# Performance work log

Hardware: AMD Instinct MI355X
Metric: run time of the kernel (lower is better)

## Reference

```python
import jax, jax.numpy as jnp
import numpy as np

L = 4        # num_layers
B = 32       # batch
N = 512      # num_nodes == seq_len
D = 256      # d_model
H = 8        # nhead
HD = D // H  # head_dim
F = 1024     # dim_feedforward
EPS = 1e-5


def setup_inputs() -> dict:
    key = jax.random.key(0)
    ks = jax.random.split(key, 12)
    w = lambda k, shape: jax.random.normal(k, shape, jnp.float32) * 0.02
    return {
        "src": jax.random.normal(ks[0], (B, N, D), jnp.float32),
        # node embeddings (torch.randn -> std 1)
        "e1": jax.random.normal(ks[1], (N, D), jnp.float32),
        "e2": jax.random.normal(ks[2], (N, D), jnp.float32),
        # per-layer attention projections, stored [L, d_in, d_out]
        "Wq": w(ks[3], (L, D, D)), "bq": jnp.zeros((L, D), jnp.float32),
        "Wk": w(ks[4], (L, D, D)), "bk": jnp.zeros((L, D), jnp.float32),
        "Wv": w(ks[5], (L, D, D)), "bv": jnp.zeros((L, D), jnp.float32),
        "Wo": w(ks[6], (L, D, D)), "bo": jnp.zeros((L, D), jnp.float32),
        # FFN
        "W1": w(ks[7], (L, D, F)), "b1": jnp.zeros((L, F), jnp.float32),
        "W2": w(ks[8], (L, F, D)), "b2": jnp.zeros((L, D), jnp.float32),
        # LayerNorms
        "g1": jnp.ones((L, D), jnp.float32), "be1": jnp.zeros((L, D), jnp.float32),
        "g2": jnp.ones((L, D), jnp.float32), "be2": jnp.zeros((L, D), jnp.float32),
    }


def _layernorm(x, g, b):
    mu = jnp.mean(x, axis=-1, keepdims=True)
    var = jnp.mean(jnp.square(x - mu), axis=-1, keepdims=True)
    return (x - mu) * jax.lax.rsqrt(var + EPS) * g + b


def reference(src, e1, e2, Wq, bq, Wk, bk, Wv, bv, Wo, bo,
              W1, b1, W2, b2, g1, be1, g2, be2):
    # adaptive spatial bias shared across all layers: [N, N]
    bias = jnp.matmul(e1, e2.T)
    scale = 1.0 / jnp.sqrt(jnp.float32(HD))
    x = src
    for l in range(L):
        def heads(t):  # [B,N,D] -> [B,H,N,HD]
            return t.reshape(B, N, H, HD).transpose(0, 2, 1, 3)
        q = heads(x @ Wq[l] + bq[l])
        k = heads(x @ Wk[l] + bk[l])
        v = heads(x @ Wv[l] + bv[l])
        # scores + shared additive bias (broadcast over batch and heads)
        scores = jnp.einsum('bhqd,bhkd->bhqk', q, k) * scale + bias
        attn = jax.nn.softmax(scores, axis=-1)
        o = jnp.einsum('bhqk,bhkd->bhqd', attn, v)
        o = o.transpose(0, 2, 1, 3).reshape(B, N, D) @ Wo[l] + bo[l]
        x = _layernorm(x + o, g1[l], be1[l])
        ff = jax.nn.relu(x @ W1[l] + b1[l]) @ W2[l] + b2[l]
        x = _layernorm(x + ff, g2[l], be2[l])
    return x
```

## Files before the change

### kernel.cpp

```cpp
#include <hip/hip_runtime.h>

typedef __bf16 bf16;
typedef __bf16 v4bf __attribute__((ext_vector_type(4)));
typedef __bf16 v8bf __attribute__((ext_vector_type(8)));
typedef float  v4f  __attribute__((ext_vector_type(4)));
typedef float  v16f __attribute__((ext_vector_type(16)));
typedef unsigned short u16;
typedef u16 v8us __attribute__((ext_vector_type(8)));
typedef unsigned int v4u __attribute__((ext_vector_type(4)));
typedef _Float16 f16;
typedef f16 v4h __attribute__((ext_vector_type(4)));

#define L_ 4
#define B_ 32
#define N_ 512
#define D_ 256
#define H_ 8
#define F_ 1024
#define ROWS (B_*N_)
#define QHSZ ((size_t)B_*H_*N_*32)

__device__ __forceinline__ void gload16(const void* g, void* l) {
  __builtin_amdgcn_global_load_lds((__attribute__((address_space(1))) void*)g,
                                   (__attribute__((address_space(3))) void*)l,
                                   16, 0, 0);
}

__device__ __forceinline__ unsigned pk_bf16(float a, float b) {
  unsigned r;
  asm("v_cvt_pk_bf16_f32 %0, %1, %2" : "=v"(r) : "v"(a), "v"(b));
  return r;
}

#define PLSWAP(a, b) asm volatile("v_permlane32_swap_b32 %0, %1" : "+v"(a), "+v"(b))

#define EXP2(x) __builtin_amdgcn_exp2f(x)

__device__ __forceinline__ unsigned encf(float f) {
  unsigned u = __float_as_uint(f);
  return (u & 0x80000000u) ? ~u : (u | 0x80000000u);
}
__device__ __forceinline__ float decf(unsigned e) {
  unsigned b = (e & 0x80000000u) ? (e & 0x7fffffffu) : ~e;
  return __uint_as_float(b);
}

template <int N> __device__ __forceinline__ void waitvm() {
  if constexpr (N == 0) asm volatile("s_waitcnt vmcnt(0)" ::: "memory");
  else if constexpr (N == 2) asm volatile("s_waitcnt vmcnt(2)" ::: "memory");
  else if constexpr (N == 3) asm volatile("s_waitcnt vmcnt(3)" ::: "memory");
  else if constexpr (N == 4) asm volatile("s_waitcnt vmcnt(4)" ::: "memory");
  else if constexpr (N == 5) asm volatile("s_waitcnt vmcnt(5)" ::: "memory");
  else if constexpr (N == 6) asm volatile("s_waitcnt vmcnt(6)" ::: "memory");
}

__global__ __launch_bounds__(256) void bias_gemm(
    const float* __restrict__ eK, const float* __restrict__ eQ,
    float* __restrict__ biasP, unsigned* __restrict__ mqe) {
  __shared__ float As[32][17];
  __shared__ float Bs[32][17];
  __shared__ float pm[16][32];
  const int tx = threadIdx.x, ty = threadIdx.y;
  const int t = ty * 16 + tx;
  const int lrow = t >> 3, lkq = (t & 7) * 2;
  const int r0 = blockIdx.y * 32, c0 = blockIdx.x * 32;
  float acc[2][2] = {{0.f, 0.f}, {0.f, 0.f}};
  for (int k0 = 0; k0 < D_; k0 += 16) {
    const float2 a2 = *(const float2*)&eK[(size_t)(r0 + lrow) * D_ + k0 + lkq];
    const float2 b2 = *(const float2*)&eQ[(size_t)(c0 + lrow) * D_ + k0 + lkq];
    As[lrow][lkq] = a2.x; As[lrow][lkq + 1] = a2.y;
    Bs[lrow][lkq] = b2.x; Bs[lrow][lkq + 1] = b2.y;
    __syncthreads();
#pragma unroll
    for (int k = 0; k < 16; ++k) {
      const float a0 = As[ty * 2][k], a1 = As[ty * 2 + 1][k];
      const float b0 = Bs[tx * 2][k], b1 = Bs[tx * 2 + 1][k];
      acc[0][0] += a0 * b0; acc[0][1] += a0 * b1;
      acc[1][0] += a1 * b0; acc[1][1] += a1 * b1;
    }
    __syncthreads();
  }
#pragma unroll
  for (int i = 0; i < 2; ++i)
#pragma unroll
    for (int j = 0; j < 2; ++j) acc[i][j] *= 1.4426950408889634f;
#pragma unroll
  for (int i = 0; i < 2; ++i) {
    const int gr = r0 + ty * 2 + i;
    const int kb = gr >> 5, r5 = gr & 31;
    const int blk = kb * 8 + (r5 >> 3) * 2 + ((r5 >> 2) & 1);
#pragma unroll
    for (int j = 0; j < 2; ++j) {
      const int q = c0 + tx * 2 + j;
      biasP[(size_t)(blk * 512 + q) * 4 + (r5 & 3)] = acc[i][j];
    }
  }
  pm[ty][tx * 2]     = fmaxf(acc[0][0], acc[1][0]);
  pm[ty][tx * 2 + 1] = fmaxf(acc[0][1], acc[1][1]);
  __syncthreads();
  if (ty == 0) {
#pragma unroll
    for (int j = 0; j < 2; ++j) {
      float m = pm[0][tx * 2 + j];
#pragma unroll
      for (int y = 1; y < 16; ++y) m = fmaxf(m, pm[y][tx * 2 + j]);
      atomicMax(&mqe[c0 + tx * 2 + j], encf(m));
    }
  }
}

__device__ __forceinline__ void convT_tile(
    const float* __restrict__ W, bf16* __restrict__ Wt,
    int K, int N, size_t inL, size_t outL, int l, int k0, int n0, int tid,
    float (*t)[33]) {
  const int r = tid >> 5, c = tid & 31;
#pragma unroll
  for (int i = 0; i < 4; ++i)
    t[r + 8 * i][c] = W[l * inL + (size_t)(k0 + r + 8 * i) * N + n0 + c];
  __syncthreads();
#pragma unroll
  for (int i = 0; i < 4; ++i)
    Wt[l * outL + (size_t)(n0 + r + 8 * i) * K + k0 + c] = (bf16)t[c][r + 8 * i];
}

__global__ __launch_bounds__(256) void setup_all(
    const float* __restrict__ src, bf16* __restrict__ xb,
    const float* __restrict__ bq, const float* __restrict__ bk,
    const float* __restrict__ bv, float* __restrict__ bqkv,
    const float* __restrict__ Wq, const float* __restrict__ Wk,
    const float* __restrict__ Wv, const float* __restrict__ Wo,
    const float* __restrict__ W1, const float* __restrict__ W2,
    bf16* __restrict__ Wqkvt, bf16* __restrict__ Wot,
    bf16* __restrict__ W1t, bf16* __restrict__ W2t,
    const float* __restrict__ biasP, f16* __restrict__ biasH,
    const unsigned* __restrict__ mqe) {
  __shared__ float t[32][33];
  const int tid = threadIdx.x;
  int id = blockIdx.x;
  if (id < 4096) {
    const int i = id * 256 + tid;
    float4 v = ((const float4*)src)[i];
    uint2 w;
    w.x = pk_bf16(v.x, v.y);
    w.y = pk_bf16(v.z, v.w);
    ((uint2*)xb)[i] = w;
    return;
  }
  id -= 4096;
  if (id < 12) {
    const int i = id * 256 + tid;
    if (i < L_ * 768) {
      const int l = i / 768, n = i - l * 768;
      float v = (n < 256) ? bq[l * 256 + n]
              : (n < 512) ? bk[l * 256 + n - 256]
                          : bv[l * 256 + n - 512];
      bqkv[i] = v;
    }
    return;
  }
  id -= 12;
  if (id < 1024) {
    const int w = id >> 8, tt = id & 255;
    const int l = tt >> 6, tile = tt & 63;
    const int n0 = (tile & 7) * 32, k0 = (tile >> 3) * 32;
    const float* W = (w == 0) ? Wq : (w == 1) ? Wk : (w == 2) ? Wv : Wo;
    bf16* Wt = (w == 3) ? Wot : (Wqkvt + w * 65536);
    const size_t outL = (w == 3) ? 65536 : 196608;
    convT_tile(W, Wt, 256, 256, 65536, outL, l, k0, n0, tid, t);
    return;
  }
  id -= 1024;
  if (id < 1024) {
    const int l = id >> 8, tile = id & 255;
    const int n0 = (tile & 31) * 32, k0 = (tile >> 5) * 32;
    convT_tile(W1, W1t, 256, 1024, 262144, 262144, l, k0, n0, tid, t);
    return;
  }
  id -= 1024;
  if (id < 1024) {
    const int l = id >> 8, tile = id & 255;
    const int n0 = (tile & 7) * 32, k0 = (tile >> 3) * 32;
    convT_tile(W2, W2t, 1024, 256, 262144, 262144, l, k0, n0, tid, t);
    return;
  }
  id -= 1024;
  {
    const int i = id * 256 + tid;
    const float4 v = ((const float4*)biasP)[i];
    const float m = decf(mqe[i & 511]);
    v4h o;
    o[0] = (f16)(v.x - m); o[1] = (f16)(v.y - m);
    o[2] = (f16)(v.z - m); o[3] = (f16)(v.w - m);
    *(v4h*)&biasH[(size_t)i * 4] = o;
  }
}

template <int BM, int BN, int WPC, int RELU, int OUTMODE, int RESID>
__global__ __launch_bounds__(256, WPC) void gemm_bf16k(
    const bf16* __restrict__ A, const bf16* __restrict__ Bt,
    const float* __restrict__ bias, const bf16* __restrict__ resid,
    void* __restrict__ Cout, int M, int N, int K, int nbx) {
  constexpr int MR = BM / 32, NR = BN / 32;
  constexpr int NSLAB = (BM + BN) / 16;
  constexpr int LPW = NSLAB / 4;
  constexpr int BUFE = (BM + BN) * 32;
  __shared__ __align__(16) bf16 lds[3 * BUFE];
  const int tid  = threadIdx.x;
  const int wave = tid >> 6, lane = tid & 63;
  const int l15 = lane & 15, l4 = lane >> 4;
  const int qq = gridDim.x >> 3;
  const int wg = (blockIdx.x & 7) * qq + (blockIdx.x >> 3);
  const int bx = wg % nbx, by = wg / nbx;
  const int bm = by * BM, bn = bx * BN;
  const int wr = (wave >> 1) * (BM / 2), wc = (wave & 1) * (BN / 2);
  const int lrow = lane >> 2;
  const int lk   = (lane & 3) * 8;

  v4f acc[MR][NR];
#pragma unroll
  for (int m = 0; m < MR; ++m)
#pragma unroll
    for (int n = 0; n < NR; ++n) acc[m][n] = (v4f){0.f, 0.f, 0.f, 0.f};

  auto STAGE = [&](int buf, int k0) {
    bf16* dst = &lds[buf * BUFE];
#pragma unroll
    for (int s = wave; s < NSLAB; s += 4) {
      if (s < BM / 16)
        gload16(A + (size_t)(bm + s * 16 + lrow) * K + k0 + lk, dst + s * 512);
      else
        gload16(Bt + (size_t)(bn + (s - BM / 16) * 16 + lrow) * K + k0 + lk, dst + s * 512);
    }
  };

  const int nk = K >> 5;
  STAGE(0, 0);
  STAGE(1, 32);
  waitvm<LPW>();
  __builtin_amdgcn_s_barrier();
  __builtin_amdgcn_sched_barrier(0);

  int cur = 0;
  for (int t = 0; t < nk; ++t) {
    const bool pf = (t + 2 < nk);
    if (pf) STAGE(cur == 0 ? 2 : cur - 1, (t + 2) * 32);
    const bf16* buf = &lds[cur * BUFE];
    v8bf af[MR], bfr[NR];
#pragma unroll
    for (int m = 0; m < MR; ++m)
      af[m] = *(const v8bf*)&buf[(wr + m * 16 + l15) * 32 + l4 * 8];
#pragma unroll
    for (int n = 0; n < NR; ++n)
      bfr[n] = *(const v8bf*)&buf[BM * 32 + (wc + n * 16 + l15) * 32 + l4 * 8];
    __builtin_amdgcn_s_setprio(1);
#pragma unroll
    for (int m = 0; m < MR; ++m)
#pragma unroll
      for (int n = 0; n < NR; ++n)
        acc[m][n] = __builtin_amdgcn_mfma_f32_16x16x32_bf16(af[m], bfr[n], acc[m][n], 0, 0, 0);
    __builtin_amdgcn_s_setprio(0);
    if (pf) waitvm<LPW>();
    else    waitvm<0>();
    __builtin_amdgcn_s_barrier();
    __builtin_amdgcn_sched_barrier(0);
    cur = (cur == 2) ? 0 : cur + 1;
  }

#pragma unroll
  for (int m = 0; m < MR; ++m) {
    const int row0 = bm + wr + m * 16 + l4 * 4;
#pragma unroll
    for (int n = 0; n < NR; ++n) {
      const int col = bn + wc + n * 16 + l15;
      const float bc = bias[col];
      if constexpr (OUTMODE == 2) {
        const int sec = col >> 8, hh = (col >> 5) & 7, d = col & 31;
        const int bb = row0 >> 9, nr0 = row0 & 511;
        bf16* dst = (bf16*)Cout + (size_t)sec * QHSZ +
                    (((size_t)bb * 8 + hh) * 512 + nr0) * 32 + d;
#pragma unroll
        for (int i = 0; i < 4; ++i)
          dst[i * 32] = (bf16)(acc[m][n][i] + bc);
      } else {
#pragma unroll
        for (int i = 0; i < 4; ++i) {
          const size_t idx = (size_t)(row0 + i) * N + col;
          float v = acc[m][n][i] + bc;
          if (RESID) v += (float)resid[idx];
          if (RELU) v = fmaxf(v, 0.f);
          if (OUTMODE == 1) ((bf16*)Cout)[idx] = (bf16)v;
          else              ((float*)Cout)[idx] = v;
        }
      }
    }
  }
}

#define VTS 520
__global__ __launch_bounds__(512, 2) void attn_k(
    const bf16* __restrict__ qkvh, const f16* __restrict__ biasH,
    bf16* __restrict__ outp) {
  __shared__ u16 Vt[32 * VTS];
  const int tid = threadIdx.x;
  const int wave = tid >> 6, lane = tid & 63;
  const int l31 = lane & 31, hi = lane >> 5;
  const int fid = blockIdx.x;
  const int xcd = fid & 7, idx = fid >> 3;
  const int b = (xcd << 2) | (idx >> 4);
  const int h = (idx >> 1) & 7;
  const int qhalf = idx & 1;
  const u16* Qh = (const u16*)qkvh + (((size_t)b * 8 + h) * 512) * 32;
  const u16* Kh = Qh + QHSZ;
  const u16* Vh = Qh + 2 * QHSZ;
  const int qb = qhalf * 256 + wave * 32;

  {
    const u16* p0 = Vh + (size_t)tid * 32;
#pragma unroll
    for (int d0 = 0; d0 < 32; d0 += 8) {
      v8us a = *(const v8us*)(p0 + d0);
#pragma unroll
      for (int j = 0; j < 8; ++j)
        Vt[(d0 + j) * VTS + tid] = a[j];
    }
  }
  __syncthreads();

  const u16* qrow = Qh + (size_t)(qb + l31) * 32;
  const v8bf qf0 = *(const v8bf*)(qrow + hi * 8);
  const v8bf qf1 = *(const v8bf*)(qrow + 16 + hi * 8);
  const f16* bpl = biasH + ((size_t)(hi * 512 + qb + l31)) * 4;

  const float SC2 = 0.17677669529663688f * 1.4426950408889634f;
  float lsum = 0.f;
  v16f accO = {0.f,0.f,0.f,0.f,0.f,0.f,0.f,0.f,0.f,0.f,0.f,0.f,0.f,0.f,0.f,0.f};

  v8bf ka0 = *(const v8bf*)(Kh + (size_t)l31 * 32 + hi * 8);
  v8bf ka1 = *(const v8bf*)(Kh + (size_t)l31 * 32 + 16 + hi * 8);
  v4h bb[4];
#pragma unroll
  for (int g = 0; g < 4; ++g) bb[g] = *(const v4h*)(bpl + (size_t)(g * 2) * 2048);

  v16f stC = {0.f,0.f,0.f,0.f,0.f,0.f,0.f,0.f,0.f,0.f,0.f,0.f,0.f,0.f,0.f,0.f};
  stC = __builtin_amdgcn_mfma_f32_32x32x16_bf16(ka0, qf0, stC, 0, 0, 0);
  stC = __builtin_amdgcn_mfma_f32_32x32x16_bf16(ka1, qf1, stC, 0, 0, 0);
  {
    const u16* kn = Kh + (size_t)(32 + l31) * 32;
    ka0 = *(const v8bf*)(kn + hi * 8);
    ka1 = *(const v8bf*)(kn + 16 + hi * 8);
  }

  for (int kb = 0; kb < 16; ++kb) {
    const int kbase = kb * 32;
    v16f stN = {0.f,0.f,0.f,0.f,0.f,0.f,0.f,0.f,0.f,0.f,0.f,0.f,0.f,0.f,0.f,0.f};
    __builtin_amdgcn_s_setprio(1);
    stN = __builtin_amdgcn_mfma_f32_32x32x16_bf16(ka0, qf0, stN, 0, 0, 0);
    stN = __builtin_amdgcn_mfma_f32_32x32x16_bf16(ka1, qf1, stN, 0, 0, 0);
    __builtin_amdgcn_s_setprio(0);

    const u16* kn = Kh + (size_t)(kbase + 64 + l31) * 32;
    const v8bf kn0 = *(const v8bf*)(kn + hi * 8);
    const v8bf kn1 = *(const v8bf*)(kn + 16 + hi * 8);
    v4h bn[4];
#pragma unroll
    for (int g = 0; g < 4; ++g)
      bn[g] = *(const v4h*)(bpl + (size_t)((kb + 1) * 8 + g * 2) * 2048);

    float p[16];
#pragma unroll
    for (int r = 0; r < 16; ++r)
      p[r] = EXP2(fmaf(stC[r], SC2, (float)bb[r >> 2][r & 3]));

    float s8[8], s4[4];
#pragma unroll
    for (int r = 0; r < 8; ++r) s8[r] = p[r] + p[r + 8];
#pragma unroll
    for (int r = 0; r < 4; ++r) s4[r] = s8[r] + s8[r + 4];
    lsum += (s4[0] + s4[2]) + (s4[1] + s4[3]);

    unsigned u[8];
#pragma unroll
    for (int t = 0; t < 8; ++t) u[t] = pk_bf16(p[2 * t], p[2 * t + 1]);
    PLSWAP(u[0], u[2]);
    PLSWAP(u[1], u[3]);
    PLSWAP(u[4], u[6]);
    PLSWAP(u[5], u[7]);
    union { v4u u; v8bf h; } cv0, cv1;
    cv0.u = (v4u){u[0], u[1], u[2], u[3]};
    cv1.u = (v4u){u[4], u[5], u[6], u[7]};

    const v8bf va0 = *(const v8bf*)&Vt[l31 * VTS + kbase + hi * 8];
    const v8bf va1 = *(const v8bf*)&Vt[l31 * VTS + kbase + 16 + hi * 8];
    __builtin_amdgcn_s_setprio(1);
    accO = __builtin_amdgcn_mfma_f32_32x32x16_bf16(va0, cv0.h, accO, 0, 0, 0);
    accO = __builtin_amdgcn_mfma_f32_32x32x16_bf16(va1, cv1.h, accO, 0, 0, 0);
    __builtin_amdgcn_s_setprio(0);

    stC = stN;
    ka0 = kn0; ka1 = kn1;
#pragma unroll
    for (int g = 0; g < 4; ++g) bb[g] = bn[g];
  }

  lsum += __shfl_xor(lsum, 32);

  const float inv = 1.0f / lsum;
  u16* orow = (u16*)outp + (size_t)(b * N_ + qb + l31) * D_ + h * 32 + 4 * hi;
#pragma unroll
  for (int g = 0; g < 4; ++g) {
    uint2 w;
    w.x = pk_bf16(accO[4 * g] * inv, accO[4 * g + 1] * inv);
    w.y = pk_bf16(accO[4 * g + 2] * inv, accO[4 * g + 3] * inv);
    *(uint2*)(orow + 8 * g) = w;
  }
}

template <int MODE>
__global__ __launch_bounds__(256) void ln_kernel(
    const float* __restrict__ xin,
    const float* __restrict__ g, const float* __restrict__ b,
    float* __restrict__ xout_f32, bf16* __restrict__ xbout) {
  const int wv = threadIdx.x >> 6, ln = threadIdx.x & 63;
  const size_t row0 = ((size_t)(blockIdx.x & 7) << 11) + (size_t)(blockIdx.x >> 3) * 8 + wv * 2;
  const size_t oA = row0 * D_ + ln * 4;
  const size_t oB = oA + D_;
  const float4 vA = *(const float4*)&xin[oA];
  const float4 vB = *(const float4*)&xin[oB];
  float sA  = (vA.x + vA.y) + (vA.z + vA.w);
  float ssA = (vA.x * vA.x + vA.y * vA.y) + (vA.z * vA.z + vA.w * vA.w);
  float sB  = (vB.x + vB.y) + (vB.z + vB.w);
  float ssB = (vB.x * vB.x + vB.y * vB.y) + (vB.z * vB.z + vB.w * vB.w);
#pragma unroll
  for (int off = 1; off < 64; off <<= 1) {
    sA  += __shfl_xor(sA, off);
    ssA += __shfl_xor(ssA, off);
    sB  += __shfl_xor(sB, off);
    ssB += __shfl_xor(ssB, off);
  }
  const float muA = sA * (1.f / D_);
  const float muB = sB * (1.f / D_);
  const float rsA = rsqrtf(ssA * (1.f / D_) - muA * muA + 1e-5f);
  const float rsB = rsqrtf(ssB * (1.f / D_) - muB * muB + 1e-5f);
  const float4 gg = *(const float4*)&g[ln * 4];
  const float4 bb = *(const float4*)&b[ln * 4];
  float4 oAv, oBv;
  oAv.x = (vA.x - muA) * rsA * gg.x + bb.x;
  oAv.y = (vA.y - muA) * rsA * gg.y + bb.y;
  oAv.z = (vA.z - muA) * rsA * gg.z + bb.z;
  oAv.w = (vA.w - muA) * rsA * gg.w + bb.w;
  oBv.x = (vB.x - muB) * rsB * gg.x + bb.x;
  oBv.y = (vB.y - muB) * rsB * gg.y + bb.y;
  oBv.z = (vB.z - muB) * rsB * gg.z + bb.z;
  oBv.w = (vB.w - muB) * rsB * gg.w + bb.w;
  if constexpr (MODE == 1) {
    *(float4*)&xout_f32[oA] = oAv;
    *(float4*)&xout_f32[oB] = oBv;
  } else {
    uint2 wA, wB;
    wA.x = pk_bf16(oAv.x, oAv.y);
    wA.y = pk_bf16(oAv.z, oAv.w);
    wB.x = pk_bf16(oBv.x, oBv.y);
    wB.y = pk_bf16(oBv.z, oBv.w);
    *(uint2*)&xbout[oA] = wA;
    *(uint2*)&xbout[oB] = wB;
  }
}

extern "C" void kernel_launch(void* const* d_in, const int* in_sizes, int n_in,
                              void* d_out, int out_size, void* d_ws, size_t ws_size,
                              hipStream_t stream) {
  const float* src = (const float*)d_in[0];
  const float* e1  = (const float*)d_in[1];
  const float* e2  = (const float*)d_in[2];
  const float* Wq  = (const float*)d_in[3];
  const float* bq  = (const float*)d_in[4];
  const float* Wk  = (const float*)d_in[5];
  const float* bk  = (const float*)d_in[6];
  const float* Wv  = (const float*)d_in[7];
  const float* bv  = (const float*)d_in[8];
  const float* Wo  = (const float*)d_in[9];
  const float* bo  = (const float*)d_in[10];
  const float* W1  = (const float*)d_in[11];
  const float* b1  = (const float*)d_in[12];
  const float* W2  = (const float*)d_in[13];
  const float* b2  = (const float*)d_in[14];
  const float* g1  = (const float*)d_in[15];
  const float* be1 = (const float*)d_in[16];
  const float* g2  = (const float*)d_in[17];
  const float* be2 = (const float*)d_in[18];

  char* ws = (char*)d_ws;
  size_t off = 0;
  auto alloc = [&](size_t bytes) {
    void* p = ws + off;
    off += (bytes + 255) & ~(size_t)255;
    return p;
  };
  float*    biasP  = (float*)alloc((size_t)1024 * 1024 + 4096);
  f16*      biasH  = (f16*)  alloc((size_t)2 * 1024 * 1024);
  unsigned* mqe    = (unsigned*)alloc((size_t)N_ * 4);
  bf16*     xb     = (bf16*) alloc((size_t)ROWS * D_ * 2);
  bf16*     attn_o = (bf16*) alloc((size_t)ROWS * D_ * 2);
  float*    tmpf   = (float*)alloc((size_t)ROWS * D_ * 4);
  bf16*     qkvh   = (bf16*) alloc((size_t)ROWS * 1024 * 2 + 65536);
  bf16*     h1     = qkvh;
  bf16*     Wqkvt  = (bf16*) alloc((size_t)L_ * 768 * 256 * 2);
  bf16*     Wot    = (bf16*) alloc((size_t)L_ * 256 * 256 * 2);
  bf16*     W1t    = (bf16*) alloc((size_t)L_ * 1024 * 256 * 2);
  bf16*     W2t    = (bf16*) alloc((size_t)L_ * 256 * 1024 * 2);
  float*    bqkv   = (float*)alloc((size_t)L_ * 768 * 4);

  hipMemsetAsync(mqe, 0, (size_t)N_ * 4, stream);
  bias_gemm<<<dim3(16, 16), dim3(16, 16), 0, stream>>>(e2, e1, biasP, mqe);
  setup_all<<<7436, 256, 0, stream>>>(
      src, xb, bq, bk, bv, bqkv,
      Wq, Wk, Wv, Wo, W1, W2, Wqkvt, Wot, W1t, W2t, biasP, biasH, mqe);

  for (int l = 0; l < L_; ++l) {
    gemm_bf16k<128, 128, 3, 0, 2, 0><<<768, 256, 0, stream>>>(
        xb, Wqkvt + (size_t)l * 196608, bqkv + l * 768, nullptr, qkvh,
        ROWS, 768, 256, 6);
    attn_k<<<512, 512, 0, stream>>>(qkvh, biasH, attn_o);
    gemm_bf16k<64, 128, 4, 0, 0, 1><<<512, 256, 0, stream>>>(
        attn_o, Wot + (size_t)l * 65536, bo + l * 256, xb, tmpf,
        ROWS, 256, 256, 2);
    ln_kernel<0><<<ROWS / 8, 256, 0, stream>>>(tmpf, g1 + l * 256, be1 + l * 256, nullptr, xb);
    gemm_bf16k<128, 256, 2, 1, 1, 0><<<512, 256, 0, stream>>>(
        xb, W1t + (size_t)l * 262144, b1 + l * 1024, nullptr, h1,
        ROWS, 1024, 256, 4);
    gemm_bf16k<64, 128, 4, 0, 0, 1><<<512, 256, 0, stream>>>(
        h1, W2t + (size_t)l * 262144, b2 + l * 256, xb, tmpf,
        ROWS, 256, 1024, 2);
    if (l == L_ - 1)
      ln_kernel<1><<<ROWS / 8, 256, 0, stream>>>(tmpf, g2 + l * 256, be2 + l * 256, (float*)d_out, nullptr);
    else
      ln_kernel<0><<<ROWS / 8, 256, 0, stream>>>(tmpf, g2 + l * 256, be2 + l * 256, nullptr, xb);
  }
}
```

Before: 392.3 us.

## Split FFN along hidden dim into two halves with accumulating second GEMM

The FFN is computed in two chunks of 512 hidden units. Each chunk runs the W1 GEMM on half the columns, then a W2 GEMM with K=512; the second W2 pass adds into the fp32 tmpf buffer through a new ACC mode. Leading-dimension parameters let the GEMM read strided halves of h1 and W2t. The W1 GEMM tile also changes from 128x256 to 128x128 with three waves per CU. The aim is better cache residency of the h1 intermediate, at the cost of two extra launches and an extra fp32 read-modify-write of tmpf.

```diff
diff --git a/kernel.cpp b/kernel.cpp
--- a/kernel.cpp
+++ b/kernel.cpp
@@ -195,11 +195,11 @@
   }
 }
 
-template <int BM, int BN, int WPC, int RELU, int OUTMODE, int RESID>
+template <int BM, int BN, int WPC, int RELU, int OUTMODE, int RESID, int ACC>
 __global__ __launch_bounds__(256, WPC) void gemm_bf16k(
     const bf16* __restrict__ A, const bf16* __restrict__ Bt,
     const float* __restrict__ bias, const bf16* __restrict__ resid,
-    void* __restrict__ Cout, int M, int N, int K, int nbx) {
+    void* __restrict__ Cout, int M, int N, int K, int nbx, int lda, int ldb) {
   constexpr int MR = BM / 32, NR = BN / 32;
   constexpr int NSLAB = (BM + BN) / 16;
   constexpr int LPW = NSLAB / 4;
@@ -227,9 +227,9 @@
 #pragma unroll
     for (int s = wave; s < NSLAB; s += 4) {
       if (s < BM / 16)
-        gload16(A + (size_t)(bm + s * 16 + lrow) * K + k0 + lk, dst + s * 512);
+        gload16(A + (size_t)(bm + s * 16 + lrow) * lda + k0 + lk, dst + s * 512);
       else
-        gload16(Bt + (size_t)(bn + (s - BM / 16) * 16 + lrow) * K + k0 + lk, dst + s * 512);
+        gload16(Bt + (size_t)(bn + (s - BM / 16) * 16 + lrow) * ldb + k0 + lk, dst + s * 512);
     }
   };
 
@@ -272,7 +272,7 @@
 #pragma unroll
     for (int n = 0; n < NR; ++n) {
       const int col = bn + wc + n * 16 + l15;
-      const float bc = bias[col];
+      const float bc = (bias != nullptr) ? bias[col] : 0.f;
       if constexpr (OUTMODE == 2) {
         const int sec = col >> 8, hh = (col >> 5) & 7, d = col & 31;
         const int bb = row0 >> 9, nr0 = row0 & 511;
@@ -287,6 +287,7 @@
           const size_t idx = (size_t)(row0 + i) * N + col;
           float v = acc[m][n][i] + bc;
           if (RESID) v += (float)resid[idx];
+          if (ACC) v += ((const float*)Cout)[idx];
           if (RELU) v = fmaxf(v, 0.f);
           if (OUTMODE == 1) ((bf16*)Cout)[idx] = (bf16)v;
           else              ((float*)Cout)[idx] = v;
@@ -517,20 +518,26 @@
       Wq, Wk, Wv, Wo, W1, W2, Wqkvt, Wot, W1t, W2t, biasP, biasH, mqe);
 
   for (int l = 0; l < L_; ++l) {
-    gemm_bf16k<128, 128, 3, 0, 2, 0><<<768, 256, 0, stream>>>(
+    gemm_bf16k<128, 128, 3, 0, 2, 0, 0><<<768, 256, 0, stream>>>(
         xb, Wqkvt + (size_t)l * 196608, bqkv + l * 768, nullptr, qkvh,
-        ROWS, 768, 256, 6);
+        ROWS, 768, 256, 6, 256, 256);
     attn_k<<<512, 512, 0, stream>>>(qkvh, biasH, attn_o);
-    gemm_bf16k<64, 128, 4, 0, 0, 1><<<512, 256, 0, stream>>>(
+    gemm_bf16k<64, 128, 4, 0, 0, 1, 0><<<512, 256, 0, stream>>>(
         attn_o, Wot + (size_t)l * 65536, bo + l * 256, xb, tmpf,
-        ROWS, 256, 256, 2);
+        ROWS, 256, 256, 2, 256, 256);
     ln_kernel<0><<<ROWS / 8, 256, 0, stream>>>(tmpf, g1 + l * 256, be1 + l * 256, nullptr, xb);
-    gemm_bf16k<128, 256, 2, 1, 1, 0><<<512, 256, 0, stream>>>(
+    gemm_bf16k<128, 128, 3, 1, 1, 0, 0><<<512, 256, 0, stream>>>(
         xb, W1t + (size_t)l * 262144, b1 + l * 1024, nullptr, h1,
-        ROWS, 1024, 256, 4);
-    gemm_bf16k<64, 128, 4, 0, 0, 1><<<512, 256, 0, stream>>>(
+        ROWS, 1024, 256, 4, 256, 256);
+    gemm_bf16k<64, 128, 4, 0, 0, 1, 0><<<512, 256, 0, stream>>>(
         h1, W2t + (size_t)l * 262144, b2 + l * 256, xb, tmpf,
-        ROWS, 256, 1024, 2);
+        ROWS, 256, 512, 2, 1024, 1024);
+    gemm_bf16k<128, 128, 3, 1, 1, 0, 0><<<512, 256, 0, stream>>>(
+        xb, W1t + (size_t)l * 262144 + 131072, b1 + l * 1024 + 512, nullptr, h1 + 512,
+        ROWS, 1024, 256, 4, 256, 256);
+    gemm_bf16k<64, 128, 4, 0, 0, 0, 1><<<512, 256, 0, stream>>>(
+        h1 + 512, W2t + (size_t)l * 262144 + 512, nullptr, nullptr, tmpf,
+        ROWS, 256, 512, 2, 1024, 1024);
     if (l == L_ - 1)
       ln_kernel<1><<<ROWS / 8, 256, 0, stream>>>(tmpf, g2 + l * 256, be2 + l * 256, (float*)d_out, nullptr);
     else
```

New measurement: 479.7 us. +22.3%, slower.
